# Optimization experiments

Hardware: AMD Instinct MI355X
Metric: run time of the kernel (lower is better)

Reference implementation:

```python
import jax, jax.numpy as jnp
import numpy as np

H = 8          # kv heads
D = 128        # head dim
EPS = 1e-6
NEG = -1e9

def rmsnorm(x, w):
    rms = jnp.sqrt(jnp.mean(x * x, axis=-1, keepdims=True) + EPS)
    return x / rms * w

def apply_rotary(x, cos, sin):
    # x: [B, h, T, D]; cos/sin: [1, 1, T, D/2]
    x1, x2 = jnp.split(x, 2, axis=-1)
    return jnp.concatenate([x1 * cos - x2 * sin, x1 * sin + x2 * cos], axis=-1)


def setup_inputs() -> dict:
    key = jax.random.key(0)
    ks = jax.random.split(key, 7)
    B, T, hid = 1, 4096, 1024
    s = 0.02
    return {
        "x":   jax.random.normal(ks[0], (B, T, hid), jnp.float32),
        "cos": jax.random.normal(ks[1], (1, 1, T, D // 2), jnp.float32),
        "sin": jax.random.normal(ks[2], (1, 1, T, D // 2), jnp.float32),
        "Wq":  jax.random.normal(ks[3], (hid, 2 * hid), jnp.float32) * s,
        "Wk":  jax.random.normal(ks[4], (hid, hid), jnp.float32) * s,
        "Wv":  jax.random.normal(ks[5], (hid, hid), jnp.float32) * s,
        "Wo":  jax.random.normal(ks[6], (2 * hid, hid), jnp.float32) * s,
        "qn_w": jnp.ones((D,), jnp.float32),
        "kn_w": jnp.ones((D,), jnp.float32),
    }


def reference(x, cos, sin, Wq, Wk, Wv, Wo, qn_w, kn_w):
    B, T, _ = x.shape
    scale = D ** -0.5

    q = (x @ Wq).reshape(B, T, 2 * H, D).transpose(0, 2, 1, 3)  # [B,2H,T,D]
    k = (x @ Wk).reshape(B, T, H, D).transpose(0, 2, 1, 3)      # [B,H,T,D]
    v = (x @ Wv).reshape(B, T, H, D).transpose(0, 2, 1, 3)      # [B,H,T,D]

    q = apply_rotary(rmsnorm(q, qn_w), cos, sin)
    k = apply_rotary(rmsnorm(k, kn_w), cos, sin)

    # GQA expand: query head i uses kv head i // 2
    k = jnp.repeat(k, 2, axis=1)  # [B,2H,T,D]
    v = jnp.repeat(v, 2, axis=1)

    attn = jnp.einsum("bhtd,bhsd->bhts", q, k) * scale
    causal = jnp.tril(jnp.ones((T, T), bool))
    attn = jnp.where(causal, attn, NEG)
    attn = jax.nn.softmax(attn, axis=-1)

    out = jnp.einsum("bhts,bhsd->bhtd", attn, v)
    out = out.transpose(0, 2, 1, 3).reshape(B, T, 2 * H * D)
    return out @ Wo
```

## Files before the change

kernel.cpp:

```cpp
#include <hip/hip_runtime.h>
#include <hip/hip_bf16.h>

#define H2 16
#define HKV 8
#define DHEAD 128
#define HID 1024
#define NQ 2048

typedef unsigned short u16;
typedef __bf16 bf16x8 __attribute__((ext_vector_type(8)));
typedef float f32x4 __attribute__((ext_vector_type(4)));

__device__ __forceinline__ u16 f2bf(float x) {
    unsigned int u = __float_as_uint(x);
    unsigned int r = (u + 0x7fffu + ((u >> 16) & 1u)) >> 16;
    return (u16)r;
}

__device__ __forceinline__ unsigned int pack_bf16(float hi, float lo) {
    unsigned int a = __float_as_uint(hi) + 0x8000u;
    unsigned int b = __float_as_uint(lo) + 0x8000u;
    return __builtin_amdgcn_perm(a, b, 0x07060302u);
}

__device__ __forceinline__ bf16x8 ld_frag(const u16* p) {
    bf16x8 r;
    *reinterpret_cast<uint4*>(&r) = *reinterpret_cast<const uint4*>(p);
    return r;
}

__device__ __forceinline__ void gload_lds16(const u16* g, u16* l) {
    __builtin_amdgcn_global_load_lds((const __attribute__((address_space(1))) void*)g,
                                     (__attribute__((address_space(3))) void*)l, 16, 0, 0);
}

__global__ __launch_bounds__(256) void cast_f32_bf16(const float* __restrict__ in,
                                                     u16* __restrict__ out, int n4) {
    int i = blockIdx.x * 256 + threadIdx.x;
    if (i < n4) {
        float4 v = reinterpret_cast<const float4*>(in)[i];
        ushort4 o;
        o.x = f2bf(v.x); o.y = f2bf(v.y); o.z = f2bf(v.z); o.w = f2bf(v.w);
        reinterpret_cast<ushort4*>(out)[i] = o;
    }
}

__global__ __launch_bounds__(256) void transpose_cast(const float* __restrict__ in,
                                                      u16* __restrict__ out, int K, int N) {
    __shared__ u16 t[32][34];
    int k0 = blockIdx.x * 32, n0 = blockIdx.y * 32;
    for (int c = threadIdx.x; c < 1024; c += 256) {
        int k = c >> 5, n = c & 31;
        t[k][n] = f2bf(in[(size_t)(k0 + k) * N + n0 + n]);
    }
    __syncthreads();
    for (int c = threadIdx.x; c < 1024; c += 256) {
        int n = c >> 5, k = c & 31;
        out[(size_t)(n0 + n) * K + k0 + k] = t[k][n];
    }
}

__global__ __launch_bounds__(256) void gemm_bf16(const u16* __restrict__ A,
                                                 const u16* __restrict__ Bt,
                                                 float* __restrict__ C,
                                                 int M, int N, int K) {
    __shared__ u16 As[128 * 32];
    __shared__ u16 Bs[128 * 32];
    int tid = threadIdx.x;
    int lane = tid & 63, wave = tid >> 6;
    int quad = lane >> 4, l15 = lane & 15;
    int wr = wave >> 1, wc = wave & 1;
    int m0 = blockIdx.y * 128, n0 = blockIdx.x * 128;

    f32x4 zero = {0.f, 0.f, 0.f, 0.f};
    f32x4 acc[4][4];
    for (int i = 0; i < 4; i++)
        for (int j = 0; j < 4; j++) acc[i][j] = zero;

    int r0 = 16 * wave + (lane >> 2);
    int r1 = r0 + 64;
    int ks0 = (lane & 3) ^ ((r0 >> 1) & 3);
    int ks1 = (lane & 3) ^ ((r1 >> 1) & 3);
    const u16* ga0 = A + (size_t)(m0 + r0) * K + ks0 * 8;
    const u16* ga1 = A + (size_t)(m0 + r1) * K + ks1 * 8;
    const u16* gb0 = Bt + (size_t)(n0 + r0) * K + ks0 * 8;
    const u16* gb1 = Bt + (size_t)(n0 + r1) * K + ks1 * 8;
    u16* la0 = &As[wave * 512];
    u16* la1 = &As[(wave + 4) * 512];
    u16* lb0 = &Bs[wave * 512];
    u16* lb1 = &Bs[(wave + 4) * 512];

    int swz = (quad ^ ((l15 >> 1) & 3)) * 8;

    for (int k0 = 0; k0 < K; k0 += 32) {
        __syncthreads();
        gload_lds16(ga0 + k0, la0);
        gload_lds16(ga1 + k0, la1);
        gload_lds16(gb0 + k0, lb0);
        gload_lds16(gb1 + k0, lb1);
        __syncthreads();
        bf16x8 a[4], b[4];
        #pragma unroll
        for (int i = 0; i < 4; i++) a[i] = ld_frag(&As[(64 * wr + 16 * i + l15) * 32 + swz]);
        #pragma unroll
        for (int j = 0; j < 4; j++) b[j] = ld_frag(&Bs[(64 * wc + 16 * j + l15) * 32 + swz]);
        #pragma unroll
        for (int i = 0; i < 4; i++)
            #pragma unroll
            for (int j = 0; j < 4; j++)
                acc[i][j] = __builtin_amdgcn_mfma_f32_16x16x32_bf16(a[i], b[j], acc[i][j], 0, 0, 0);
    }
    for (int i = 0; i < 4; i++) {
        int rowb = m0 + 64 * wr + 16 * i + quad * 4;
        for (int j = 0; j < 4; j++) {
            int col = n0 + 64 * wc + 16 * j + l15;
            for (int r = 0; r < 4; r++)
                C[(size_t)(rowb + r) * N + col] = acc[i][j][r];
        }
    }
}

__global__ __launch_bounds__(256) void norm_rope(const float* __restrict__ raw,
                                                 const float* __restrict__ cosp,
                                                 const float* __restrict__ sinp,
                                                 const float* __restrict__ w,
                                                 u16* __restrict__ out,
                                                 int T, int nh, int rowstride, int coloff,
                                                 float outscale) {
    int wave = threadIdx.x >> 6, lane = threadIdx.x & 63;
    int wid = blockIdx.x * 4 + wave;
    int t = wid / nh, h = wid % nh;
    if (t >= T) return;
    const float* r = raw + (size_t)t * rowstride + coloff + h * 128;
    float v1 = r[lane], v2 = r[lane + 64];
    float ss = v1 * v1 + v2 * v2;
    for (int off = 1; off < 64; off <<= 1) ss += __shfl_xor(ss, off);
    float inv = rsqrtf(ss * (1.f / 128.f) + 1e-6f);
    float n1 = v1 * inv * w[lane], n2 = v2 * inv * w[lane + 64];
    float c = cosp[(size_t)t * 64 + lane], s = sinp[(size_t)t * 64 + lane];
    float o1 = (n1 * c - n2 * s) * outscale;
    float o2 = (n1 * s + n2 * c) * outscale;
    u16* op = out + ((size_t)h * T + t) * 128;
    op[lane] = f2bf(o1);
    op[lane + 64] = f2bf(o2);
}

__global__ __launch_bounds__(256) void v_transpose(const float* __restrict__ vraw,
                                                   u16* __restrict__ Vbt, int T) {
    __shared__ u16 tt[128][72];
    int h = blockIdx.y, t0 = blockIdx.x * 64;
    for (int c = threadIdx.x; c < 8192; c += 256) {
        int r = c >> 7, d = c & 127;
        tt[d][r] = f2bf(vraw[(size_t)(t0 + r) * 4096 + 3072 + h * 128 + d]);
    }
    __syncthreads();
    for (int c = threadIdx.x; c < 8192; c += 256) {
        int d = c >> 6, r = c & 63;
        Vbt[((size_t)h * 128 + d) * T + t0 + r] = tt[d][r];
    }
}

__global__ __launch_bounds__(256) void flash_attn(const u16* __restrict__ Qb,
                                                  const u16* __restrict__ Kb,
                                                  const u16* __restrict__ Vbt,
                                                  u16* __restrict__ attn, int T) {
    __shared__ u16 Ks[2][64 * 128];
    __shared__ u16 Vt[2][128 * 64];
    __shared__ u16 Ps[64 * 64];
    int tid = threadIdx.x;
    int lane = tid & 63, wave = tid >> 6;
    int quad = lane >> 4, l15 = lane & 15;
    int swb8 = (l15 & 7) * 8;
    int h = blockIdx.y;
    int j = (int)blockIdx.x;
    int kvh = h >> 1;

    const u16* kbase = Kb + (size_t)kvh * T * 128;
    const u16* vbase = Vbt + (size_t)kvh * 128 * T;

    int krow_ = (lane >> 4);
    int kseg_ = (lane & 15);
    int vrow_ = (lane >> 3);
    int vseg_ = (lane & 7);

    auto stage = [&](int s0, int b) {
        #pragma unroll
        for (int i = 0; i < 4; i++) {
            int ch = wave * 4 + i;
            int r = ch * 4 + krow_;
            int s = kseg_ ^ (r & 7);
            gload_lds16(kbase + (size_t)(s0 + r) * 128 + s * 8, &Ks[b][ch * 512]);
        }
        #pragma unroll
        for (int i = 0; i < 4; i++) {
            int ch = wave * 4 + i;
            int d = ch * 8 + vrow_;
            int s = vseg_ ^ (d & 7);
            gload_lds16(vbase + (size_t)d * T + s0 + s * 8, &Vt[b][ch * 512]);
        }
    };

    bf16x8 onesf;
    #pragma unroll
    for (int i = 0; i < 8; i++) onesf[i] = (__bf16)1.0f;
    f32x4 zero = {0.f, 0.f, 0.f, 0.f};
    const float L2E = 1.44269504f;

    for (int pass = 0; pass < 2; ++pass) {
        int qt = pass == 0 ? (63 - j) : j;
        int q0 = qt * 64;

        bf16x8 qf[4];
        {
            const u16* qp = Qb + ((size_t)h * T + q0 + 16 * wave + l15) * 128 + quad * 8;
            #pragma unroll
            for (int kk = 0; kk < 4; kk++) qf[kk] = ld_frag(qp + kk * 32);
        }

        float m_i = -3.0e38f;
        f32x4 lsum = zero;
        f32x4 o[8];
        for (int dt = 0; dt < 8; dt++) o[dt] = zero;

        int ntiles = qt + 1;
        stage(0, 0);
        __syncthreads();

        for (int it = 0; it < ntiles; ++it) {
            int b = it & 1;
            if (it + 1 < ntiles) stage((it + 1) * 64, 1 - b);
            int s0 = it * 64;

            f32x4 scT[4];
            for (int jt = 0; jt < 4; jt++) scT[jt] = zero;
            #pragma unroll
            for (int kk = 0; kk < 4; kk++)
                #pragma unroll
                for (int jt = 0; jt < 4; jt++) {
                    bf16x8 kfrag = ld_frag(&Ks[b][(jt * 16 + l15) * 128 + ((kk * 32 + quad * 8) ^ swb8)]);
                    scT[jt] = __builtin_amdgcn_mfma_f32_16x16x32_bf16(kfrag, qf[kk], scT[jt], 0, 0, 0);
                }

            if (s0 == q0) {
                int qloc = 16 * wave + l15;
                #pragma unroll
                for (int jt = 0; jt < 4; jt++)
                    for (int r = 0; r < 4; r++)
                        if (jt * 16 + quad * 4 + r > qloc) scT[jt][r] = -1e30f;
            }

            float mt = scT[0][0];
            #pragma unroll
            for (int jt = 0; jt < 4; jt++)
                for (int r = 0; r < 4; r++) mt = fmaxf(mt, scT[jt][r]);
            mt = fmaxf(mt, __shfl_xor(mt, 16));
            mt = fmaxf(mt, __shfl_xor(mt, 32));
            float mnew = fmaxf(m_i, mt);
            float alpha = __expf(m_i - mnew);
            m_i = mnew;
            float mls = mnew * L2E;

            #pragma unroll
            for (int jt = 0; jt < 4; jt++)
                for (int r = 0; r < 4; r++)
                    scT[jt][r] = exp2f(fmaf(scT[jt][r], L2E, -mls));

            {
                int prow = 16 * wave + l15;
                #pragma unroll
                for (int jt = 0; jt < 4; jt++) {
                    int s8 = 2 * jt + (quad >> 1);
                    uint2 wv;
                    wv.x = pack_bf16(scT[jt][1], scT[jt][0]);
                    wv.y = pack_bf16(scT[jt][3], scT[jt][2]);
                    *reinterpret_cast<uint2*>(&Ps[prow * 64 + (s8 ^ (l15 & 7)) * 8 + (quad & 1) * 4]) = wv;
                }
            }

            float av[4];
            #pragma unroll
            for (int r = 0; r < 4; r++) av[r] = __shfl(alpha, quad * 4 + r);
            #pragma unroll
            for (int r = 0; r < 4; r++) lsum[r] *= av[r];
            #pragma unroll
            for (int dt = 0; dt < 8; dt++)
                for (int r = 0; r < 4; r++) o[dt][r] *= av[r];

            asm volatile("s_waitcnt lgkmcnt(0)" ::: "memory");

            #pragma unroll
            for (int kk2 = 0; kk2 < 2; kk2++) {
                bf16x8 pa = ld_frag(&Ps[(16 * wave + l15) * 64 + (((4 * kk2 + quad) ^ (l15 & 7)) * 8)]);
                lsum = __builtin_amdgcn_mfma_f32_16x16x32_bf16(pa, onesf, lsum, 0, 0, 0);
                #pragma unroll
                for (int dt = 0; dt < 8; dt++) {
                    bf16x8 vb = ld_frag(&Vt[b][(dt * 16 + l15) * 64 + ((kk2 * 32 + quad * 8) ^ swb8)]);
                    o[dt] = __builtin_amdgcn_mfma_f32_16x16x32_bf16(pa, vb, o[dt], 0, 0, 0);
                }
            }
            __syncthreads();
        }

        float inv[4];
        for (int r = 0; r < 4; r++) inv[r] = 1.f / lsum[r];
        for (int dt = 0; dt < 8; dt++)
            for (int r = 0; r < 4; r++) {
                int row = q0 + 16 * wave + quad * 4 + r;
                attn[(size_t)row * NQ + h * DHEAD + dt * 16 + l15] = f2bf(o[dt][r] * inv[r]);
            }
    }
}

extern "C" void kernel_launch(void* const* d_in, const int* in_sizes, int n_in,
                              void* d_out, int out_size, void* d_ws, size_t ws_size,
                              hipStream_t stream) {
    const float* x    = (const float*)d_in[0];
    const float* cosp = (const float*)d_in[1];
    const float* sinp = (const float*)d_in[2];
    const float* Wq   = (const float*)d_in[3];
    const float* Wk   = (const float*)d_in[4];
    const float* Wv   = (const float*)d_in[5];
    const float* Wo   = (const float*)d_in[6];
    const float* qnw  = (const float*)d_in[7];
    const float* knw  = (const float*)d_in[8];
    float* out = (float*)d_out;
    const int T = in_sizes[1] / 64;

    char* ws = (char*)d_ws;
    size_t off = 0;
    auto alloc = [&](size_t bytes) {
        char* p = ws + off;
        off += (bytes + 255) & ~(size_t)255;
        return p;
    };
    u16*   xb     = (u16*)alloc((size_t)T * HID * 2);
    u16*   Wqkvb  = (u16*)alloc((size_t)4096 * HID * 2);
    u16*   Wob    = (u16*)alloc((size_t)HID * NQ * 2);
    float* qkvraw = (float*)alloc((size_t)T * 4096 * 4);
    u16*   Qb     = (u16*)alloc((size_t)H2 * T * DHEAD * 2);
    u16*   Kb     = (u16*)alloc((size_t)HKV * T * DHEAD * 2);
    u16*   Vbt    = (u16*)alloc((size_t)HKV * DHEAD * T * 2);
    u16*   attn   = (u16*)alloc((size_t)T * NQ * 2);

    cast_f32_bf16<<<(T * HID / 4 + 255) / 256, 256, 0, stream>>>(x, xb, T * HID / 4);
    transpose_cast<<<dim3(HID / 32, NQ / 32), 256, 0, stream>>>(Wq, Wqkvb, HID, NQ);
    transpose_cast<<<dim3(HID / 32, HID / 32), 256, 0, stream>>>(Wk, Wqkvb + (size_t)2048 * HID, HID, HID);
    transpose_cast<<<dim3(HID / 32, HID / 32), 256, 0, stream>>>(Wv, Wqkvb + (size_t)3072 * HID, HID, HID);
    transpose_cast<<<dim3(NQ / 32, HID / 32), 256, 0, stream>>>(Wo, Wob, NQ, HID);

    gemm_bf16<<<dim3(4096 / 128, T / 128), 256, 0, stream>>>(xb, Wqkvb, qkvraw, T, 4096, HID);

    const float scale = 0.08838834764831845f;
    norm_rope<<<T * H2 / 4, 256, 0, stream>>>(qkvraw, cosp, sinp, qnw, Qb, T, H2, 4096, 0, scale);
    norm_rope<<<T * HKV / 4, 256, 0, stream>>>(qkvraw, cosp, sinp, knw, Kb, T, HKV, 4096, 2048, 1.0f);
    v_transpose<<<dim3(T / 64, HKV), 256, 0, stream>>>(qkvraw, Vbt, T);

    flash_attn<<<dim3(32, H2), 256, 0, stream>>>(Qb, Kb, Vbt, attn, T);

    gemm_bf16<<<dim3(HID / 128, T / 128), 256, 0, stream>>>(attn, Wob, out, T, HID, NQ);
}
```

Before: 377.5 us.

## Fuse paired causal query tiles into one pass sharing K/V tile loads

Each block now handles its two query tiles (63-j and j) together in a single loop over KV tiles. Each staged K/V tile is reused for both tiles while the shorter one is still active, so the shared prefix is loaded only once, and the second pass's reload is gone. It also skips the O/lsum rescale when no lane's running max changed, and adds a second P buffer plus a minimum of 2 blocks per CU in launch bounds. In exchange, holding two sets of accumulators raises register pressure, which with the occupancy hint may cause spills, and the per-iteration branches on doB add divergence-free but extra control flow.

```diff
diff --git a/kernel.cpp b/kernel.cpp
--- a/kernel.cpp
+++ b/kernel.cpp
@@ -160,13 +160,13 @@
     }
 }
 
-__global__ __launch_bounds__(256) void flash_attn(const u16* __restrict__ Qb,
-                                                  const u16* __restrict__ Kb,
-                                                  const u16* __restrict__ Vbt,
-                                                  u16* __restrict__ attn, int T) {
+__global__ __launch_bounds__(256, 2) void flash_attn(const u16* __restrict__ Qb,
+                                                     const u16* __restrict__ Kb,
+                                                     const u16* __restrict__ Vbt,
+                                                     u16* __restrict__ attn, int T) {
     __shared__ u16 Ks[2][64 * 128];
     __shared__ u16 Vt[2][128 * 64];
-    __shared__ u16 Ps[64 * 64];
+    __shared__ u16 Ps[2][64 * 64];
     int tid = threadIdx.x;
     int lane = tid & 63, wave = tid >> 6;
     int quad = lane >> 4, l15 = lane & 15;
@@ -175,6 +175,10 @@
     int j = (int)blockIdx.x;
     int kvh = h >> 1;
 
+    int qa = 63 - j, qb = j;
+    int nA = qa + 1, nB = qb + 1;
+    int q0a = qa * 64, q0b = qb * 64;
+
     const u16* kbase = Kb + (size_t)kvh * T * 128;
     const u16* vbase = Vbt + (size_t)kvh * 128 * T;
 
@@ -206,107 +210,160 @@
     f32x4 zero = {0.f, 0.f, 0.f, 0.f};
     const float L2E = 1.44269504f;
 
-    for (int pass = 0; pass < 2; ++pass) {
-        int qt = pass == 0 ? (63 - j) : j;
-        int q0 = qt * 64;
-
-        bf16x8 qf[4];
-        {
-            const u16* qp = Qb + ((size_t)h * T + q0 + 16 * wave + l15) * 128 + quad * 8;
-            #pragma unroll
-            for (int kk = 0; kk < 4; kk++) qf[kk] = ld_frag(qp + kk * 32);
-        }
-
-        float m_i = -3.0e38f;
-        f32x4 lsum = zero;
-        f32x4 o[8];
-        for (int dt = 0; dt < 8; dt++) o[dt] = zero;
-
-        int ntiles = qt + 1;
-        stage(0, 0);
-        __syncthreads();
-
-        for (int it = 0; it < ntiles; ++it) {
-            int b = it & 1;
-            if (it + 1 < ntiles) stage((it + 1) * 64, 1 - b);
-            int s0 = it * 64;
-
-            f32x4 scT[4];
-            for (int jt = 0; jt < 4; jt++) scT[jt] = zero;
+    bf16x8 qfA[4], qfB[4];
+    {
+        const u16* qpA = Qb + ((size_t)h * T + q0a + 16 * wave + l15) * 128 + quad * 8;
+        const u16* qpB = Qb + ((size_t)h * T + q0b + 16 * wave + l15) * 128 + quad * 8;
+        #pragma unroll
+        for (int kk = 0; kk < 4; kk++) { qfA[kk] = ld_frag(qpA + kk * 32); qfB[kk] = ld_frag(qpB + kk * 32); }
+    }
+
+    float mA = -3.0e38f, mB = -3.0e38f;
+    f32x4 lsumA = zero, lsumB = zero;
+    f32x4 oA[8], oB[8];
+    for (int dt = 0; dt < 8; dt++) { oA[dt] = zero; oB[dt] = zero; }
+
+    int qloc = 16 * wave + l15;
+
+    auto softmax_upd = [&](f32x4 sc[4], float& mi) -> float {
+        float mt = sc[0][0];
+        #pragma unroll
+        for (int jt = 0; jt < 4; jt++)
+            for (int r = 0; r < 4; r++) mt = fmaxf(mt, sc[jt][r]);
+        mt = fmaxf(mt, __shfl_xor(mt, 16));
+        mt = fmaxf(mt, __shfl_xor(mt, 32));
+        float mnew = fmaxf(mi, mt);
+        float alpha = __expf(mi - mnew);
+        mi = mnew;
+        float mls = mnew * L2E;
+        #pragma unroll
+        for (int jt = 0; jt < 4; jt++)
+            for (int r = 0; r < 4; r++)
+                sc[jt][r] = exp2f(fmaf(sc[jt][r], L2E, -mls));
+        return alpha;
+    };
+    auto ps_write = [&](u16* P, f32x4 sc[4]) {
+        int prow = 16 * wave + l15;
+        #pragma unroll
+        for (int jt = 0; jt < 4; jt++) {
+            int s8 = 2 * jt + (quad >> 1);
+            uint2 wv;
+            wv.x = pack_bf16(sc[jt][1], sc[jt][0]);
+            wv.y = pack_bf16(sc[jt][3], sc[jt][2]);
+            *reinterpret_cast<uint2*>(&P[prow * 64 + (s8 ^ (l15 & 7)) * 8 + (quad & 1) * 4]) = wv;
+        }
+    };
+    auto rescale = [&](float alpha, f32x4& lsum, f32x4 o[8]) {
+        if (__any(alpha != 1.0f)) {
+            float av[4];
+            #pragma unroll
+            for (int r = 0; r < 4; r++) av[r] = __shfl(alpha, quad * 4 + r);
+            #pragma unroll
+            for (int r = 0; r < 4; r++) lsum[r] *= av[r];
+            #pragma unroll
+            for (int dt = 0; dt < 8; dt++)
+                for (int r = 0; r < 4; r++) o[dt][r] *= av[r];
+        }
+    };
+
+    stage(0, 0);
+    __syncthreads();
+
+    for (int i = 0; i < nA; ++i) {
+        int b = i & 1;
+        if (i + 1 < nA) stage((i + 1) * 64, 1 - b);
+        bool doB = (i < nB);
+
+        f32x4 scA[4], scB[4];
+        for (int jt = 0; jt < 4; jt++) { scA[jt] = zero; scB[jt] = zero; }
+
+        if (doB) {
             #pragma unroll
             for (int kk = 0; kk < 4; kk++)
                 #pragma unroll
                 for (int jt = 0; jt < 4; jt++) {
                     bf16x8 kfrag = ld_frag(&Ks[b][(jt * 16 + l15) * 128 + ((kk * 32 + quad * 8) ^ swb8)]);
-                    scT[jt] = __builtin_amdgcn_mfma_f32_16x16x32_bf16(kfrag, qf[kk], scT[jt], 0, 0, 0);
+                    scA[jt] = __builtin_amdgcn_mfma_f32_16x16x32_bf16(kfrag, qfA[kk], scA[jt], 0, 0, 0);
+                    scB[jt] = __builtin_amdgcn_mfma_f32_16x16x32_bf16(kfrag, qfB[kk], scB[jt], 0, 0, 0);
                 }
-
-            if (s0 == q0) {
-                int qloc = 16 * wave + l15;
+        } else {
+            #pragma unroll
+            for (int kk = 0; kk < 4; kk++)
                 #pragma unroll
-                for (int jt = 0; jt < 4; jt++)
-                    for (int r = 0; r < 4; r++)
-                        if (jt * 16 + quad * 4 + r > qloc) scT[jt][r] = -1e30f;
-            }
-
-            float mt = scT[0][0];
-            #pragma unroll
-            for (int jt = 0; jt < 4; jt++)
-                for (int r = 0; r < 4; r++) mt = fmaxf(mt, scT[jt][r]);
-            mt = fmaxf(mt, __shfl_xor(mt, 16));
-            mt = fmaxf(mt, __shfl_xor(mt, 32));
-            float mnew = fmaxf(m_i, mt);
-            float alpha = __expf(m_i - mnew);
-            m_i = mnew;
-            float mls = mnew * L2E;
-
+                for (int jt = 0; jt < 4; jt++) {
+                    bf16x8 kfrag = ld_frag(&Ks[b][(jt * 16 + l15) * 128 + ((kk * 32 + quad * 8) ^ swb8)]);
+                    scA[jt] = __builtin_amdgcn_mfma_f32_16x16x32_bf16(kfrag, qfA[kk], scA[jt], 0, 0, 0);
+                }
+        }
+
+        if (i == nA - 1) {
             #pragma unroll
             for (int jt = 0; jt < 4; jt++)
                 for (int r = 0; r < 4; r++)
-                    scT[jt][r] = exp2f(fmaf(scT[jt][r], L2E, -mls));
-
-            {
-                int prow = 16 * wave + l15;
-                #pragma unroll
-                for (int jt = 0; jt < 4; jt++) {
-                    int s8 = 2 * jt + (quad >> 1);
-                    uint2 wv;
-                    wv.x = pack_bf16(scT[jt][1], scT[jt][0]);
-                    wv.y = pack_bf16(scT[jt][3], scT[jt][2]);
-                    *reinterpret_cast<uint2*>(&Ps[prow * 64 + (s8 ^ (l15 & 7)) * 8 + (quad & 1) * 4]) = wv;
-                }
-            }
-
-            float av[4];
-            #pragma unroll
-            for (int r = 0; r < 4; r++) av[r] = __shfl(alpha, quad * 4 + r);
-            #pragma unroll
-            for (int r = 0; r < 4; r++) lsum[r] *= av[r];
-            #pragma unroll
-            for (int dt = 0; dt < 8; dt++)
-                for (int r = 0; r < 4; r++) o[dt][r] *= av[r];
-
-            asm volatile("s_waitcnt lgkmcnt(0)" ::: "memory");
-
+                    if (jt * 16 + quad * 4 + r > qloc) scA[jt][r] = -1e30f;
+        }
+        if (doB && i == nB - 1) {
+            #pragma unroll
+            for (int jt = 0; jt < 4; jt++)
+                for (int r = 0; r < 4; r++)
+                    if (jt * 16 + quad * 4 + r > qloc) scB[jt][r] = -1e30f;
+        }
+
+        float alphaA = softmax_upd(scA, mA);
+        ps_write(Ps[0], scA);
+        float alphaB = 1.0f;
+        if (doB) {
+            alphaB = softmax_upd(scB, mB);
+            ps_write(Ps[1], scB);
+        }
+
+        rescale(alphaA, lsumA, oA);
+        if (doB) rescale(alphaB, lsumB, oB);
+
+        asm volatile("s_waitcnt lgkmcnt(0)" ::: "memory");
+
+        if (doB) {
             #pragma unroll
             for (int kk2 = 0; kk2 < 2; kk2++) {
-                bf16x8 pa = ld_frag(&Ps[(16 * wave + l15) * 64 + (((4 * kk2 + quad) ^ (l15 & 7)) * 8)]);
-                lsum = __builtin_amdgcn_mfma_f32_16x16x32_bf16(pa, onesf, lsum, 0, 0, 0);
+                bf16x8 paA = ld_frag(&Ps[0][(16 * wave + l15) * 64 + (((4 * kk2 + quad) ^ (l15 & 7)) * 8)]);
+                bf16x8 paB = ld_frag(&Ps[1][(16 * wave + l15) * 64 + (((4 * kk2 + quad) ^ (l15 & 7)) * 8)]);
+                lsumA = __builtin_amdgcn_mfma_f32_16x16x32_bf16(paA, onesf, lsumA, 0, 0, 0);
+                lsumB = __builtin_amdgcn_mfma_f32_16x16x32_bf16(paB, onesf, lsumB, 0, 0, 0);
                 #pragma unroll
                 for (int dt = 0; dt < 8; dt++) {
                     bf16x8 vb = ld_frag(&Vt[b][(dt * 16 + l15) * 64 + ((kk2 * 32 + quad * 8) ^ swb8)]);
-                    o[dt] = __builtin_amdgcn_mfma_f32_16x16x32_bf16(pa, vb, o[dt], 0, 0, 0);
+                    oA[dt] = __builtin_amdgcn_mfma_f32_16x16x32_bf16(paA, vb, oA[dt], 0, 0, 0);
+                    oB[dt] = __builtin_amdgcn_mfma_f32_16x16x32_bf16(paB, vb, oB[dt], 0, 0, 0);
                 }
             }
-            __syncthreads();
-        }
-
+        } else {
+            #pragma unroll
+            for (int kk2 = 0; kk2 < 2; kk2++) {
+                bf16x8 paA = ld_frag(&Ps[0][(16 * wave + l15) * 64 + (((4 * kk2 + quad) ^ (l15 & 7)) * 8)]);
+                lsumA = __builtin_amdgcn_mfma_f32_16x16x32_bf16(paA, onesf, lsumA, 0, 0, 0);
+                #pragma unroll
+                for (int dt = 0; dt < 8; dt++) {
+                    bf16x8 vb = ld_frag(&Vt[b][(dt * 16 + l15) * 64 + ((kk2 * 32 + quad * 8) ^ swb8)]);
+                    oA[dt] = __builtin_amdgcn_mfma_f32_16x16x32_bf16(paA, vb, oA[dt], 0, 0, 0);
+                }
+            }
+        }
+        __syncthreads();
+    }
+
+    {
         float inv[4];
-        for (int r = 0; r < 4; r++) inv[r] = 1.f / lsum[r];
+        for (int r = 0; r < 4; r++) inv[r] = 1.f / lsumA[r];
         for (int dt = 0; dt < 8; dt++)
             for (int r = 0; r < 4; r++) {
-                int row = q0 + 16 * wave + quad * 4 + r;
-                attn[(size_t)row * NQ + h * DHEAD + dt * 16 + l15] = f2bf(o[dt][r] * inv[r]);
+                int row = q0a + 16 * wave + quad * 4 + r;
+                attn[(size_t)row * NQ + h * DHEAD + dt * 16 + l15] = f2bf(oA[dt][r] * inv[r]);
+            }
+        for (int r = 0; r < 4; r++) inv[r] = 1.f / lsumB[r];
+        for (int dt = 0; dt < 8; dt++)
+            for (int r = 0; r < 4; r++) {
+                int row = q0b + 16 * wave + quad * 4 + r;
+                attn[(size_t)row * NQ + h * DHEAD + dt * 16 + l15] = f2bf(oB[dt][r] * inv[r]);
             }
     }
 }
```

Measured after the change: 495.3 us. 31.2% more time.
